# Kernel tuning notes

Measured on AMD Instinct MI355X. Metric: run time of the kernel, lower is better.

Reference implementation:

```python
import jax, jax.numpy as jnp
import numpy as np

INPUT_DIM = 2304
SUBSPACE_DIM = 64
ATOMS = 512
NUM_EXPERTS = 256
K = 4


def leaky_offset_relu(x, negative_slope, offset):
    return jnp.where(x >= offset, x, negative_slope * x)


def setup_inputs() -> dict:
    key = jax.random.key(0)
    k0, k1, k2, k3 = jax.random.split(key, 4)
    x = jax.random.normal(k0, (INPUT_DIM,), dtype=jnp.float32)
    # top-level autoencoder encoder (he_uniform approximated by scaled normal)
    enc_top = jax.random.normal(k1, (NUM_EXPERTS, INPUT_DIM), dtype=jnp.float32) * (1.0 / np.sqrt(INPUT_DIM))
    # per-expert down-projection, row-normalized as in __init__
    W_down = jax.random.normal(k2, (NUM_EXPERTS, SUBSPACE_DIM, INPUT_DIM), dtype=jnp.float32)
    W_down = W_down / jnp.linalg.norm(W_down, axis=-1, keepdims=True)
    # per-expert encoder weights, row-normalized as in __init__
    encoder_weights = jax.random.normal(k3, (NUM_EXPERTS, ATOMS, SUBSPACE_DIM), dtype=jnp.float32)
    encoder_weights = encoder_weights / jnp.linalg.norm(encoder_weights, axis=-1, keepdims=True)
    return {"x": x, "enc_top": enc_top, "W_down": W_down, "encoder_weights": encoder_weights}


def reference(x, enc_top, W_down, encoder_weights):
    offset_top = 1.0 / jnp.sqrt(jnp.float32(INPUT_DIM))
    # --- top-level encode: codes = relu_offset(E @ x), negative_slope=0.0 ---
    codes = leaky_offset_relu(enc_top @ x, 0.0, offset_top)  # [num_experts]
    # --- top-k routing (naive_top_k == top_k on a single row) ---
    top_k_values, top_k_indices = jax.lax.top_k(codes, K)  # [k], [k]
    # --- gather per-expert weights, dispatch, expert compute ---
    sel_W_down = W_down[top_k_indices]            # [k, sub, in]
    sel_enc = encoder_weights[top_k_indices]      # [k, atoms, sub]
    subspace_outputs = jnp.einsum('ksd,d->ks', sel_W_down, x)        # [k, sub]
    expert_codes = jnp.einsum('kas,ks->ka', sel_enc, subspace_outputs)  # [k, atoms]
    expert_codes = leaky_offset_relu(expert_codes, 0.01, offset_top)
    # --- decode: top-level decoder is encoder^T; select columns by indices ---
    top_level_output = jnp.einsum('kd,k->d', enc_top[top_k_indices], top_k_values)  # [in]
    # expert decoders are encoder^T, W_up is W_down^T (weight tying)
    decoded_subspace = jnp.einsum('kas,ka->ks', sel_enc, expert_codes)  # [k, sub]
    reconstructed = jnp.einsum('ksd,ks->d', sel_W_down, decoded_subspace)  # sum over experts -> [in]
    return reconstructed + top_level_output
```

## Files before the change

kernel.cpp:

```cpp
#include <hip/hip_runtime.h>
#include <float.h>

#define INPUT_DIM 2304
#define SUB_DIM 64
#define ATOMS 512
#define NUM_EXPERTS 256
#define TOPK 4

#define OFFSET (1.0f / 48.0f)
#define MAGIC 0x9E3779B9u

typedef unsigned long long u64;

__device__ __forceinline__ u64 pair_ld(const u64* p) {
    return __hip_atomic_load(p, __ATOMIC_RELAXED, __HIP_MEMORY_SCOPE_AGENT);
}
__device__ __forceinline__ void pair_st(u64* p, u64 v) {
    __hip_atomic_store(p, v, __ATOMIC_RELAXED, __HIP_MEMORY_SCOPE_AGENT);
}
__device__ __forceinline__ u64 pack(float f) {
    return ((u64)__float_as_uint(f) << 32) | (u64)MAGIC;
}
__device__ __forceinline__ bool pvalid(u64 v) { return (unsigned)v == MAGIC; }
__device__ __forceinline__ float payload(u64 v) { return __uint_as_float((unsigned)(v >> 32)); }
__device__ __forceinline__ float dot4(float4 a, float4 b) {
    return a.x * b.x + a.y * b.y + a.z * b.z + a.w * b.w;
}


__global__ void __launch_bounds__(256, 1) moe_fused(
    const float* __restrict__ x,
    const float* __restrict__ enc_top,
    const float* __restrict__ W_down,
    const float* __restrict__ enc_w,
    float* __restrict__ out,
    float* __restrict__ ws_f)
{
    u64* pc = (u64*)ws_f;
    u64* ps = pc + 256 * 256;
    u64* pd = ps + 4 * 256;

    __shared__ float s_red[256];
    __shared__ float s_sub[SUB_DIM];
    __shared__ float s_ec[128];
    __shared__ float s_decp[16][SUB_DIM];
    __shared__ float s_dec[SUB_DIM];
    __shared__ int   s_idx[TOPK];
    __shared__ float s_val[TOPK];

    const int b    = blockIdx.x;
    const int t    = threadIdx.x;
    const int lane = t & 63;
    const int wave = t >> 6;
    const float4* x4 = (const float4*)x;

    {
        const float4* row4 = (const float4*)(enc_top + (size_t)b * INPUT_DIM);
        float acc = dot4(row4[t], x4[t]) + dot4(row4[t + 256], x4[t + 256]);
        if (t < 64) acc += dot4(row4[t + 512], x4[t + 512]);
        #pragma unroll
        for (int o = 32; o > 0; o >>= 1) acc += __shfl_down(acc, o);
        if (lane == 0) s_red[wave] = acc;
        __syncthreads();
        float c = (s_red[0] + s_red[1]) + (s_red[2] + s_red[3]);
        c = (c >= OFFSET) ? c : 0.0f;
        pair_st(&pc[(size_t)t * 256 + b], pack(c));
    }

    if (wave == 0) {
        u64 v0, v1, v2, v3;
        for (;;) {
            v0 = pair_ld(&pc[(size_t)b * 256 + lane]);
            v1 = pair_ld(&pc[(size_t)b * 256 + lane + 64]);
            v2 = pair_ld(&pc[(size_t)b * 256 + lane + 128]);
            v3 = pair_ld(&pc[(size_t)b * 256 + lane + 192]);
            if (__all(pvalid(v0) && pvalid(v1) && pvalid(v2) && pvalid(v3))) break;
        }
        float v[4] = { payload(v0), payload(v1), payload(v2), payload(v3) };
        int   id[4] = { lane, lane + 64, lane + 128, lane + 192 };
        for (int k = 0; k < TOPK; ++k) {
            float bv = v[0]; int bi = id[0];
            #pragma unroll
            for (int i = 1; i < 4; ++i)
                if (v[i] > bv || (v[i] == bv && id[i] < bi)) { bv = v[i]; bi = id[i]; }
            #pragma unroll
            for (int o = 32; o > 0; o >>= 1) {
                float ov = __shfl_down(bv, o);
                int   oi = __shfl_down(bi, o);
                if (ov > bv || (ov == bv && oi < bi)) { bv = ov; bi = oi; }
            }
            bv = __shfl(bv, 0);
            bi = __shfl(bi, 0);
            if (lane == 0) { s_idx[k] = bi; s_val[k] = bv; }
            #pragma unroll
            for (int i = 0; i < 4; ++i)
                if (id[i] == bi) v[i] = -FLT_MAX;
        }
        pair_st(&pc[(size_t)b * 256 + lane], 0ull);
        pair_st(&pc[(size_t)b * 256 + lane + 64], 0ull);
        pair_st(&pc[(size_t)b * 256 + lane + 128], 0ull);
        pair_st(&pc[(size_t)b * 256 + lane + 192], 0ull);
    }
    __syncthreads();

    const float* Wq = nullptr;
    float pf = 0.0f;
    if (b >= 44 && b < 60) {
        const int eb = b - 44;
        const int e  = eb >> 2, q = eb & 3;
        Wq = enc_w + ((size_t)s_idx[e] * ATOMS + (size_t)q * 128) * SUB_DIM;
        float4 w0 = ((const float4*)Wq)[(size_t)(t * 2) * 4];
        float4 w1 = ((const float4*)Wq)[(size_t)(t * 2 + 1) * 4];
        pf = w0.x + w0.w + w1.x + w1.w;
    }

    {
        const int E = s_idx[b >> 6];
        const float4* row4 = (const float4*)(W_down + ((size_t)E * SUB_DIM + (b & 63)) * INPUT_DIM);
        float acc = dot4(row4[t], x4[t]) + dot4(row4[t + 256], x4[t + 256]);
        if (t < 64) acc += dot4(row4[t + 512], x4[t + 512]);
        #pragma unroll
        for (int o = 32; o > 0; o >>= 1) acc += __shfl_down(acc, o);
        if (lane == 0) s_red[wave] = acc;
        __syncthreads();
        float s = (s_red[0] + s_red[1]) + (s_red[2] + s_red[3]);
        if (t < 4) pair_st(&ps[(size_t)t * 256 + b], pack(s));
    }

    if (b < 8 || b >= 60) return;

    if (b >= 44) {
        const int eb = b - 44;
        const int e  = eb >> 2, q = eb & 3;
        if (wave == 0) {
            u64 v;
            for (;;) {
                v = pair_ld(&ps[(size_t)q * 256 + e * SUB_DIM + lane]);
                if (__all(pvalid(v))) break;
            }
            s_sub[lane] = payload(v);
            pair_st(&ps[(size_t)q * 256 + e * SUB_DIM + lane], 0ull);
        }
        asm volatile("" :: "v"(pf));
        __syncthreads();
        if (t < 128) {
            const float4* row4 = (const float4*)(Wq + (size_t)t * SUB_DIM);
            float acc = 0.0f;
            #pragma unroll
            for (int i = 0; i < SUB_DIM / 4; ++i) {
                float4 w = row4[i];
                acc += w.x * s_sub[4*i] + w.y * s_sub[4*i+1] + w.z * s_sub[4*i+2] + w.w * s_sub[4*i+3];
            }
            s_ec[t] = (acc >= OFFSET) ? acc : 0.01f * acc;
        }
        __syncthreads();
        {
            const int sg = t & 15, ch = t >> 4;
            float4 a4 = make_float4(0.f, 0.f, 0.f, 0.f);
            #pragma unroll
            for (int aa = ch * 8; aa < ch * 8 + 8; ++aa) {
                float4 w = *(const float4*)(Wq + (size_t)aa * SUB_DIM + sg * 4);
                float  ec = s_ec[aa];
                a4.x += w.x * ec; a4.y += w.y * ec; a4.z += w.z * ec; a4.w += w.w * ec;
            }
            *(float4*)&s_decp[ch][sg * 4] = a4;
        }
        __syncthreads();
        if (t < SUB_DIM) {
            float d = 0.0f;
            #pragma unroll
            for (int c = 0; c < 16; ++c) d += s_decp[c][t];
            s_dec[t] = d;
        }
        __syncthreads();
        {
            const u64 pv = pack(s_dec[lane]);
            #pragma unroll
            for (int i = 0; i < 9; ++i) {
                const int r = wave + 4 * i;
                pair_st(&pd[(((size_t)r * TOPK + e) * 4 + q) * 64 + lane], pv);
            }
        }
        return;
    }

    {
        __syncthreads();
        const int rb = b - 8;
        const int d  = rb * 64 + lane;
        const int E  = s_idx[wave];
        float wr[SUB_DIM];
        const float* Wb = W_down + (size_t)E * SUB_DIM * INPUT_DIM + d;
        #pragma unroll
        for (int s = 0; s < SUB_DIM; ++s) wr[s] = Wb[(size_t)s * INPUT_DIM];
        const float et = s_val[wave] * enc_top[(size_t)E * INPUT_DIM + d];
        const size_t base = ((size_t)rb * TOPK + wave) * 4 * 64 + lane;
        u64 v0, v1, v2, v3;
        for (;;) {
            v0 = pair_ld(&pd[base]);
            v1 = pair_ld(&pd[base + 64]);
            v2 = pair_ld(&pd[base + 128]);
            v3 = pair_ld(&pd[base + 192]);
            if (__all(pvalid(v0) && pvalid(v1) && pvalid(v2) && pvalid(v3))) break;
        }
        float dv = (payload(v0) + payload(v1)) + (payload(v2) + payload(v3));
        pair_st(&pd[base], 0ull);
        pair_st(&pd[base + 64], 0ull);
        pair_st(&pd[base + 128], 0ull);
        pair_st(&pd[base + 192], 0ull);
        float a0 = 0.f, a1 = 0.f, a2 = 0.f, a3 = 0.f;
        #pragma unroll
        for (int s = 0; s < SUB_DIM; s += 4) {
            a0 += wr[s]     * __shfl(dv, s);
            a1 += wr[s + 1] * __shfl(dv, s + 1);
            a2 += wr[s + 2] * __shfl(dv, s + 2);
            a3 += wr[s + 3] * __shfl(dv, s + 3);
        }
        s_red[t] = et + ((a0 + a1) + (a2 + a3));
        __syncthreads();
        if (t < 64)
            out[rb * 64 + t] = s_red[t] + s_red[t + 64] + s_red[t + 128] + s_red[t + 192];
    }
}

extern "C" void kernel_launch(void* const* d_in, const int* in_sizes, int n_in,
                              void* d_out, int out_size, void* d_ws, size_t ws_size,
                              hipStream_t stream) {
    const float* x       = (const float*)d_in[0];
    const float* enc_top = (const float*)d_in[1];
    const float* W_down  = (const float*)d_in[2];
    const float* enc_w   = (const float*)d_in[3];
    float* out = (float*)d_out;
    float* ws  = (float*)d_ws;

    moe_fused<<<dim3(256), dim3(256), 0, stream>>>(x, enc_top, W_down, enc_w, out, ws);
}
```

Before: 16.57 us.

## Split expert atom work across 64 blocks and drop block-level subspace reduction

The expert atom stage now runs on 64 blocks, each handling 32 atoms, where it previously used 16 blocks of 128 atoms. The down-projection partial sums are published per wave instead of being reduced through shared memory with a barrier, and consumers sum the four wave partials themselves. The decode consumers must now poll 16 partial slots instead of 4, and more workspace is used. The aim is shorter per-block critical paths in the serial expert stage, at the cost of more global flag traffic and more polling.

```diff
diff --git a/kernel.cpp b/kernel.cpp
--- a/kernel.cpp
+++ b/kernel.cpp
@@ -38,11 +38,11 @@
 {
     u64* pc = (u64*)ws_f;
     u64* ps = pc + 256 * 256;
-    u64* pd = ps + 4 * 256;
+    u64* pd = ps + 16 * 256 * 4;
 
     __shared__ float s_red[256];
     __shared__ float s_sub[SUB_DIM];
-    __shared__ float s_ec[128];
+    __shared__ float s_ec[32];
     __shared__ float s_decp[16][SUB_DIM];
     __shared__ float s_dec[SUB_DIM];
     __shared__ int   s_idx[TOPK];
@@ -105,13 +105,12 @@
 
     const float* Wq = nullptr;
     float pf = 0.0f;
-    if (b >= 44 && b < 60) {
+    if (b >= 44 && b < 108) {
         const int eb = b - 44;
-        const int e  = eb >> 2, q = eb & 3;
-        Wq = enc_w + ((size_t)s_idx[e] * ATOMS + (size_t)q * 128) * SUB_DIM;
-        float4 w0 = ((const float4*)Wq)[(size_t)(t * 2) * 4];
-        float4 w1 = ((const float4*)Wq)[(size_t)(t * 2 + 1) * 4];
-        pf = w0.x + w0.w + w1.x + w1.w;
+        const int e  = eb >> 4, q = eb & 15;
+        Wq = enc_w + ((size_t)s_idx[e] * ATOMS + (size_t)q * 32) * SUB_DIM;
+        float4 w = ((const float4*)Wq)[(size_t)(t & 127) * 4];
+        pf = w.x + w.w;
     }
 
     {
@@ -120,30 +119,34 @@
         float acc = dot4(row4[t], x4[t]) + dot4(row4[t + 256], x4[t + 256]);
         if (t < 64) acc += dot4(row4[t + 512], x4[t + 512]);
         #pragma unroll
-        for (int o = 32; o > 0; o >>= 1) acc += __shfl_down(acc, o);
-        if (lane == 0) s_red[wave] = acc;
-        __syncthreads();
-        float s = (s_red[0] + s_red[1]) + (s_red[2] + s_red[3]);
-        if (t < 4) pair_st(&ps[(size_t)t * 256 + b], pack(s));
-    }
-
-    if (b < 8 || b >= 60) return;
+        for (int o = 32; o > 0; o >>= 1) acc += __shfl_xor(acc, o);
+        if (lane < 16)
+            pair_st(&ps[((size_t)lane * 256 + b) * 4 + wave], pack(acc));
+    }
+
+    if (b < 8 || b >= 108) return;
 
     if (b >= 44) {
         const int eb = b - 44;
-        const int e  = eb >> 2, q = eb & 3;
+        const int e  = eb >> 4, q = eb & 15;
         if (wave == 0) {
-            u64 v;
+            const size_t sbase = ((size_t)q * 256 + e * SUB_DIM + lane) * 4;
+            u64 w0, w1, w2, w3;
             for (;;) {
-                v = pair_ld(&ps[(size_t)q * 256 + e * SUB_DIM + lane]);
-                if (__all(pvalid(v))) break;
-            }
-            s_sub[lane] = payload(v);
-            pair_st(&ps[(size_t)q * 256 + e * SUB_DIM + lane], 0ull);
+                w0 = pair_ld(&ps[sbase]);
+                w1 = pair_ld(&ps[sbase + 1]);
+                w2 = pair_ld(&ps[sbase + 2]);
+                w3 = pair_ld(&ps[sbase + 3]);
+                if (__all(pvalid(w0) && pvalid(w1) && pvalid(w2) && pvalid(w3))) break;
+            }
+            s_sub[lane] = (payload(w0) + payload(w1)) + (payload(w2) + payload(w3));
+            pair_st(&ps[sbase], 0ull);
+            pair_st(&ps[sbase + 1], 0ull);
+            pair_st(&ps[sbase + 2], 0ull);
+            pair_st(&ps[sbase + 3], 0ull);
         }
         asm volatile("" :: "v"(pf));
-        __syncthreads();
-        if (t < 128) {
+        if (t < 32) {
             const float4* row4 = (const float4*)(Wq + (size_t)t * SUB_DIM);
             float acc = 0.0f;
             #pragma unroll
@@ -158,7 +161,7 @@
             const int sg = t & 15, ch = t >> 4;
             float4 a4 = make_float4(0.f, 0.f, 0.f, 0.f);
             #pragma unroll
-            for (int aa = ch * 8; aa < ch * 8 + 8; ++aa) {
+            for (int aa = ch * 2; aa < ch * 2 + 2; ++aa) {
                 float4 w = *(const float4*)(Wq + (size_t)aa * SUB_DIM + sg * 4);
                 float  ec = s_ec[aa];
                 a4.x += w.x * ec; a4.y += w.y * ec; a4.z += w.z * ec; a4.w += w.w * ec;
@@ -178,14 +181,13 @@
             #pragma unroll
             for (int i = 0; i < 9; ++i) {
                 const int r = wave + 4 * i;
-                pair_st(&pd[(((size_t)r * TOPK + e) * 4 + q) * 64 + lane], pv);
+                pair_st(&pd[(((size_t)r * TOPK + e) * 16 + q) * 64 + lane], pv);
             }
         }
         return;
     }
 
     {
-        __syncthreads();
         const int rb = b - 8;
         const int d  = rb * 64 + lane;
         const int E  = s_idx[wave];
@@ -194,20 +196,30 @@
         #pragma unroll
         for (int s = 0; s < SUB_DIM; ++s) wr[s] = Wb[(size_t)s * INPUT_DIM];
         const float et = s_val[wave] * enc_top[(size_t)E * INPUT_DIM + d];
-        const size_t base = ((size_t)rb * TOPK + wave) * 4 * 64 + lane;
-        u64 v0, v1, v2, v3;
+        const size_t base = ((size_t)rb * TOPK + wave) * 16 * 64 + lane;
+        u64 v[16];
         for (;;) {
-            v0 = pair_ld(&pd[base]);
-            v1 = pair_ld(&pd[base + 64]);
-            v2 = pair_ld(&pd[base + 128]);
-            v3 = pair_ld(&pd[base + 192]);
-            if (__all(pvalid(v0) && pvalid(v1) && pvalid(v2) && pvalid(v3))) break;
-        }
-        float dv = (payload(v0) + payload(v1)) + (payload(v2) + payload(v3));
-        pair_st(&pd[base], 0ull);
-        pair_st(&pd[base + 64], 0ull);
-        pair_st(&pd[base + 128], 0ull);
-        pair_st(&pd[base + 192], 0ull);
+            bool ok = true;
+            #pragma unroll
+            for (int i = 0; i < 16; ++i) v[i] = pair_ld(&pd[base + (size_t)i * 64]);
+            #pragma unroll
+            for (int i = 0; i < 16; ++i) ok = ok && pvalid(v[i]);
+            if (__all(ok)) break;
+        }
+        float dv = 0.0f;
+        {
+            float p0 = 0.f, p1 = 0.f, p2 = 0.f, p3 = 0.f;
+            #pragma unroll
+            for (int i = 0; i < 16; i += 4) {
+                p0 += payload(v[i]);
+                p1 += payload(v[i + 1]);
+                p2 += payload(v[i + 2]);
+                p3 += payload(v[i + 3]);
+            }
+            dv = (p0 + p1) + (p2 + p3);
+        }
+        #pragma unroll
+        for (int i = 0; i < 16; ++i) pair_st(&pd[base + (size_t)i * 64], 0ull);
         float a0 = 0.f, a1 = 0.f, a2 = 0.f, a3 = 0.f;
         #pragma unroll
         for (int s = 0; s < SUB_DIM; s += 4) {
@@ -216,10 +228,11 @@
             a2 += wr[s + 2] * __shfl(dv, s + 2);
             a3 += wr[s + 3] * __shfl(dv, s + 3);
         }
-        s_red[t] = et + ((a0 + a1) + (a2 + a3));
+        float* red = (float*)s_decp;
+        red[t] = et + ((a0 + a1) + (a2 + a3));
         __syncthreads();
         if (t < 64)
-            out[rb * 64 + t] = s_red[t] + s_red[t + 64] + s_red[t + 128] + s_red[t + 192];
+            out[rb * 64 + t] = red[t] + red[t + 64] + red[t + 128] + red[t + 192];
     }
 }
 
```

After: 16.68 us. No clear change (+0.7%).
